# Kernel optimization log

Measured on AMD Instinct MI355X. Metric: run time of the kernel, lower is better.

Reference implementation:

```python
import jax, jax.numpy as jnp
import numpy as np

WIDTH = 64
MODES = 64
NBLOCKS = 4
PAD = 2
DT = 1.0
FSTRENGTH = 2.0
FORDER = 8


def _phi1(z, eps=1e-6):
    small = jnp.abs(z) < eps
    series = 1.0 + z * 0.5 + z * z / 6.0
    safe = (jnp.exp(z) - 1.0) / jnp.where(small, 1.0, z)
    return jnp.where(small, series, safe)


def _smooth_filter(m, strength, order):
    g = jnp.linspace(0.0, 1.0, m)
    r = jnp.sqrt(g * g + 1e-12)
    return jnp.exp(-strength * r ** order)


def setup_inputs() -> dict:
    key = jax.random.key(0)
    ks = jax.random.split(key, 12)
    B, X, IS, NC = 16, 16384, 10, 3
    W, M, NB = WIDTH, MODES, NBLOCKS
    H = 2 * W
    inp = {}
    inp["x"] = jax.random.normal(ks[0], (B, X, IS * NC), jnp.float32)
    inp["grid"] = jax.random.uniform(ks[1], (B, X, 1), jnp.float32)
    def lin(k, o, i):
        return jax.random.normal(k, (o, i), jnp.float32) / np.sqrt(i).astype(np.float32)
    inp["fc0_w"] = lin(ks[2], W, IS * NC + 1); inp["fc0_b"] = jnp.zeros((W,), jnp.float32)
    inp["fc1_w"] = lin(ks[3], 128, W); inp["fc1_b"] = jnp.zeros((128,), jnp.float32)
    inp["fc2_w"] = lin(ks[4], NC, 128); inp["fc2_b"] = jnp.zeros((NC,), jnp.float32)
    inp["g_w1"] = jax.random.normal(ks[5], (NB, H, W), jnp.float32) / np.sqrt(W).astype(np.float32)
    inp["g_b1"] = jnp.zeros((NB, H), jnp.float32)
    inp["g_w2"] = jax.random.normal(ks[6], (NB, W, H), jnp.float32) / np.sqrt(H).astype(np.float32)
    inp["g_b2"] = jnp.zeros((NB, W), jnp.float32)
    inp["w_w"] = jax.random.normal(ks[7], (NB, W, W), jnp.float32) / np.sqrt(W).astype(np.float32)
    inp["w_b"] = jnp.zeros((NB, W), jnp.float32)
    inp["log_decay"] = jax.random.normal(ks[8], (NB, W, M), jnp.float32) * 0.1
    scale = 1.0 / (W * W)
    inp["mix_re"] = scale * jax.random.uniform(ks[9], (NB, W, W, M), jnp.float32)
    inp["mix_im"] = scale * jax.random.uniform(ks[10], (NB, W, W, M), jnp.float32)
    inp["alpha_w_raw"] = jnp.asarray(np.log(np.expm1(0.6)), jnp.float32)
    inp["alpha_g_raw"] = jnp.asarray(np.log(np.expm1(1.0)), jnp.float32)
    return inp


def reference(x, grid, fc0_w, fc0_b, fc1_w, fc1_b, fc2_w, fc2_b,
              g_w1, g_b1, g_w2, g_b2, w_w, w_b, log_decay, mix_re, mix_im,
              alpha_w_raw, alpha_g_raw):
    gelu = lambda t: jax.nn.gelu(t, approximate=False)  # torch default GELU is exact erf
    # lift: cat grid, fc0, move channels first, pad right
    h = jnp.concatenate([x, grid], axis=-1) @ fc0_w.T + fc0_b      # [B,X,W]
    h = jnp.transpose(h, (0, 2, 1))                                 # [B,W,X]
    h = jnp.pad(h, ((0, 0), (0, 0), (0, PAD)))                      # [B,W,Xp]
    Xp = h.shape[-1]
    aw = jax.nn.softplus(alpha_w_raw)
    ag = jax.nn.softplus(alpha_g_raw)
    filt = _smooth_filter(MODES, FSTRENGTH, FORDER)                 # [M]
    for i in range(NBLOCKS):
        # pointwise MLP g(x) (1x1 convs == channel matmuls)
        gmid = gelu(jnp.einsum('oc,bcx->box', g_w1[i], h) + g_b1[i][None, :, None])
        g = ag * (jnp.einsum('oc,bcx->box', g_w2[i], gmid) + g_b2[i][None, :, None])
        # spectral ETD step
        v_hat = jnp.fft.rfft(h)                                     # [B,W,Xp//2+1] complex
        g_hat = jnp.fft.rfft(g)
        lam = -jax.nn.softplus(log_decay[i])                        # [W,M], beta=0 so real
        z = DT * lam
        expz = jnp.exp(z)[None]                                     # [1,W,M]
        phi = _phi1(z)[None]
        mix = mix_re[i] + 1j * mix_im[i]                            # [W,W,M]
        gm = jnp.einsum('bim,iom->bom', g_hat[:, :, :MODES], mix)
        out_m = expz * v_hat[:, :, :MODES] + (DT * phi * gm) * filt[None, None, :]
        out_hat = jnp.concatenate([out_m, jnp.zeros_like(v_hat[:, :, MODES:])], axis=-1)
        etd_out = jnp.fft.irfft(out_hat, n=Xp)
        # skip path: 1x1 conv, scaled (inner_steps=1 -> w_scale=1)
        wout = jnp.einsum('oc,bcx->box', w_w[i], h) + w_b[i][None, :, None]
        upd = etd_out + aw * wout
        h = upd if i == NBLOCKS - 1 else gelu(upd)
    h = h[..., :-PAD]
    h = jnp.transpose(h, (0, 2, 1))                                 # [B,X,W]
    h = gelu(h @ fc1_w.T + fc1_b)
    h = h @ fc2_w.T + fc2_b
    return h[:, :, None, :]                                         # [B,X,1,NC]
```

## Files before the change

kernel.cpp:

```cpp
#include <hip/hip_runtime.h>
#include <hip/hip_bf16.h>


#define BB 16
#define X 16384
#define XP 16386
#define XPAD 16512
#define W 64
#define H 128
#define M 64
#define NB 4
#define NC 3

typedef __hip_bfloat16 bf16;
typedef __attribute__((ext_vector_type(8))) short short8;
typedef __attribute__((ext_vector_type(4))) float floatx4;

__device__ __forceinline__ float gelu_f(float x){
  float x3 = x * x * x;
  float y2 = 1.5957691216f * x + 0.0713548162f * x3;
  float e = __expf(y2);
  float th = 1.f - 2.f / (e + 1.f);
  return 0.5f * x * (1.f + th);
}
__device__ __forceinline__ float softplus_f(float v){
  return (v > 20.f) ? v : log1pf(expf(v));
}
__device__ __forceinline__ short f2bs(float f){
  union { float f; unsigned u; } v; v.f = f;
  unsigned r = (v.u + 0x7FFFu + ((v.u >> 16) & 1u)) >> 16;
  return (short)r;
}
__device__ __forceinline__ float bs2f(short s){
  union { unsigned u; float f; } v; v.u = ((unsigned)(unsigned short)s) << 16;
  return v.f;
}
#define MFMA(a,b,c) __builtin_amdgcn_mfma_f32_16x16x32_bf16((a),(b),(c),0,0,0)

__global__ __launch_bounds__(256) void k_basisT(short* __restrict__ basT16){
  int idx = blockIdx.x * 256 + threadIdx.x;
  if (idx >= 128 * XPAD) return;
  int mp = idx / XPAD, x = idx - mp * XPAD;
  float v = 0.f;
  if (x < XP){
    int m = mp >> 1;
    int tt = (int)(((long long)x * (long long)m) % XP);
    float ang = 6.283185307179586477f * (float)tt / (float)XP;
    float s, c; sincosf(ang, &s, &c);
    v = (mp & 1) ? s : c;
  }
  basT16[idx] = f2bs(v);
}
__global__ __launch_bounds__(256) void k_basisC(short* __restrict__ basC16){
  int idx = blockIdx.x * 256 + threadIdx.x;
  if (idx >= XPAD * 128) return;
  int x = idx >> 7, kp = idx & 127;
  float v = 0.f;
  if (x < XP){
    int m = kp >> 1;
    int tt = (int)(((long long)x * (long long)m) % XP);
    float ang = 6.283185307179586477f * (float)tt / (float)XP;
    float s, c; sincosf(ang, &s, &c);
    v = (kp & 1) ? -s : c;
  }
  basC16[idx] = f2bs(v);
}

__global__ __launch_bounds__(256) void k_decay(const float* __restrict__ log_decay,
                                               float* __restrict__ expz,
                                               float* __restrict__ phi){
  int idx = blockIdx.x * 256 + threadIdx.x;
  if (idx >= NB * W * M) return;
  float z = -softplus_f(log_decay[idx]);
  expz[idx] = expf(z);
  float p;
  if (fabsf(z) < 1e-6f) p = 1.0f + 0.5f * z + z * z * (1.0f / 6.0f);
  else                  p = expm1f(z) / z;
  phi[idx] = p;
}

__global__ void k_filt(float* __restrict__ filt){
  int m = threadIdx.x;
  if (m < M){
    float g = (float)m / 63.0f;
    float r2 = g * g + 1e-12f;
    float r4 = r2 * r2;
    float r8 = r4 * r4;
    filt[m] = expf(-2.0f * r8);
  }
}

__global__ __launch_bounds__(256) void k_prep(const float* __restrict__ w_w,
                                              const float* __restrict__ g_w1,
                                              const float* __restrict__ fc1_w,
                                              const float* __restrict__ fc0_w,
                                              const float* __restrict__ awr,
                                              short* __restrict__ ww16,
                                              short* __restrict__ w116,
                                              short* __restrict__ w1fc16,
                                              short* __restrict__ w0fc16){
  int idx = blockIdx.x * 256 + threadIdx.x;
  float aw = softplus_f(awr[0]);
  if (idx < 16384){ ww16[idx] = f2bs(aw * w_w[idx]); }
  else if (idx < 49152){ int i = idx - 16384; w116[i] = f2bs(g_w1[i]); }
  else if (idx < 57344){ int i = idx - 49152; w1fc16[i] = f2bs(fc1_w[i]); }
  else if (idx < 59392){
    int i = idx - 57344;
    int o = i >> 5, f = i & 31;
    w0fc16[i] = (f < 31) ? f2bs(fc0_w[o * 31 + f]) : (short)0;
  }
}

__global__ __launch_bounds__(256) void k_fc0m(const float* __restrict__ xg,
                                              const float* __restrict__ gg,
                                              const short* __restrict__ w0fc16,
                                              const float* __restrict__ bg,
                                              short* __restrict__ h16,
                                              short* __restrict__ hX){
  __shared__ short xs16[128][40];
  __shared__ short xp[128][72];
  int b = blockIdx.y, bx = blockIdx.x, x0 = bx * 128, t = threadIdx.x;
  if (bx == 128){
    for (int i = t; i < 64 * 128; i += 256){
      int c = i >> 7, x = i & 127;
      h16[((size_t)b * 64 + c) * XPAD + x0 + x] = 0;
    }
    short8 z8 = (short8){0,0,0,0,0,0,0,0};
    for (int u = 0; u < 4; ++u){
      int idx = u * 256 + t;
      int x = idx >> 3, col = (idx & 7) * 8;
      *(short8*)&hX[((size_t)b * XPAD + x0 + x) * 64 + col] = z8;
    }
    return;
  }
  for (int i = t; i < 3840; i += 256){
    int x = i / 30, f = i - x * 30;
    xs16[x][f] = f2bs(xg[((size_t)b * X + x0 + x) * 30 + f]);
  }
  if (t < 128){ xs16[t][30] = f2bs(gg[(size_t)b * X + x0 + t]); xs16[t][31] = 0; }
  __syncthreads();
  int w = t >> 6, l = t & 63, q = l >> 4, ln = l & 15;
  floatx4 acc[4][2];
  #pragma unroll
  for (int mt = 0; mt < 4; ++mt)
    #pragma unroll
    for (int nt = 0; nt < 2; ++nt) acc[mt][nt] = (floatx4){0.f,0.f,0.f,0.f};
  #pragma unroll
  for (int mt = 0; mt < 4; ++mt){
    short8 av = *(const short8*)&w0fc16[(mt * 16 + ln) * 32 + q * 8];
    #pragma unroll
    for (int nt = 0; nt < 2; ++nt){
      short8 bv = *(const short8*)&xs16[w * 32 + nt * 16 + ln][q * 8];
      acc[mt][nt] = MFMA(av, bv, acc[mt][nt]);
    }
  }
  #pragma unroll
  for (int mt = 0; mt < 4; ++mt)
    #pragma unroll
    for (int r = 0; r < 4; ++r){
      int o = mt * 16 + q * 4 + r;
      float bias = bg[o];
      #pragma unroll
      for (int nt = 0; nt < 2; ++nt){
        int xl = w * 32 + nt * 16 + ln;
        short s = f2bs(acc[mt][nt][r] + bias);
        h16[((size_t)b * 64 + o) * XPAD + x0 + xl] = s;
        xp[xl][o] = s;
      }
    }
  __syncthreads();
  #pragma unroll
  for (int u = 0; u < 4; ++u){
    int idx = u * 256 + t;
    int x = idx >> 3, col = (idx & 7) * 8;
    *(short8*)&hX[((size_t)b * XPAD + x0 + x) * 64 + col] = *(const short8*)&xp[x][col];
  }
}

__global__ __launch_bounds__(256) void k_dft(const short* __restrict__ h16,
                                             const short* __restrict__ hX,
                                             const short* __restrict__ w116,
                                             const float* __restrict__ b1g,
                                             const short* __restrict__ basT16,
                                             float* __restrict__ vhat,
                                             float* __restrict__ gmidhat, int blk){
  __shared__ __align__(16) char smem[52224];
  short (*srcT)[136] = (short(*)[136])smem;
  short (*hT)[72]    = (short(*)[72])(smem + 17408);
  short (*basS)[136] = (short(*)[136])(smem + 17408);
  int b = blockIdx.y, z = blockIdx.z, bx = blockIdx.x, t = threadIdx.x;
  int w = t >> 6, l = t & 63, q = l >> 4, ln = l & 15;
  const short* hbase = h16 + (size_t)b * 64 * XPAD;
  const short* hXb   = hX + (size_t)b * XPAD * 64;
  floatx4 acc[8];
  #pragma unroll
  for (int i = 0; i < 8; ++i) acc[i] = (floatx4){0.f,0.f,0.f,0.f};
  short8 aw1[2];
  float bias[4];
  if (z){
    #pragma unroll
    for (int ks = 0; ks < 2; ++ks)
      aw1[ks] = *(const short8*)&w116[((size_t)blk * H + (z-1)*64 + w*16 + ln) * 64 + ks*32 + q*8];
    #pragma unroll
    for (int r = 0; r < 4; ++r)
      bias[r] = b1g[blk * H + (z-1)*64 + w*16 + q*4 + r];
  }
  for (int ci = bx; ci < 129; ci += 17){
    int xc = ci * 128;
    __syncthreads();
    if (z == 0){
      #pragma unroll
      for (int u = 0; u < 4; ++u){
        int idx = u * 256 + t;
        int c = idx >> 4, col = (idx & 15) * 8;
        *(short8*)&srcT[c][col] = *(const short8*)&hbase[(size_t)c * XPAD + xc + col];
      }
    } else {
      #pragma unroll
      for (int u = 0; u < 4; ++u){
        int idx = u * 256 + t;
        int x = idx >> 3, col = (idx & 7) * 8;
        *(short8*)&hT[x][col] = *(const short8*)&hXb[(size_t)(xc + x) * 64 + col];
      }
    }
    __syncthreads();
    if (z){
      floatx4 a2[8];
      #pragma unroll
      for (int i = 0; i < 8; ++i) a2[i] = (floatx4){0.f,0.f,0.f,0.f};
      #pragma unroll
      for (int ks = 0; ks < 2; ++ks){
        #pragma unroll
        for (int nt = 0; nt < 8; ++nt){
          short8 bv = *(const short8*)&hT[nt*16 + ln][ks*32 + q*8];
          a2[nt] = MFMA(aw1[ks], bv, a2[nt]);
        }
      }
      #pragma unroll
      for (int nt = 0; nt < 8; ++nt){
        int gx = xc + nt*16 + ln;
        #pragma unroll
        for (int r = 0; r < 4; ++r){
          int o = w*16 + q*4 + r;
          float vv = gelu_f(a2[nt][r] + bias[r]);
          srcT[o][nt*16 + ln] = (gx < XP) ? f2bs(vv) : (short)0;
        }
      }
    }
    __syncthreads();
    #pragma unroll
    for (int u = 0; u < 8; ++u){
      int idx = u * 256 + t;
      int mp = idx >> 4, col = (idx & 15) * 8;
      *(short8*)&basS[mp][col] = *(const short8*)&basT16[(size_t)mp * XPAD + xc + col];
    }
    __syncthreads();
    #pragma unroll
    for (int ks = 0; ks < 4; ++ks){
      short8 av = *(const short8*)&srcT[w*16 + ln][ks*32 + q*8];
      #pragma unroll
      for (int nt = 0; nt < 8; ++nt){
        short8 bv = *(const short8*)&basS[nt*16 + ln][ks*32 + q*8];
        acc[nt] = MFMA(av, bv, acc[nt]);
      }
    }
  }
  #pragma unroll
  for (int nt = 0; nt < 8; ++nt)
    #pragma unroll
    for (int r = 0; r < 4; ++r){
      int mp = nt*16 + ln;
      int c  = w*16 + q*4 + r;
      float v = acc[nt][r];
      if (mp & 1) v = -v;
      if (z == 0) atomicAdd(&vhat[((size_t)b * W + c) * 128 + mp], v);
      else atomicAdd(&gmidhat[((size_t)b * H + (z-1)*64 + c) * 128 + mp], v);
    }
}

__global__ __launch_bounds__(256) void k_ghat(const float* __restrict__ gmidhat,
                                              const float* __restrict__ w2g,
                                              const float* __restrict__ b2g,
                                              const float* __restrict__ agr,
                                              float* __restrict__ ghat, int blk){
  __shared__ float w2s[64][133];
  int b = blockIdx.x, zg = blockIdx.y, t = threadIdx.x;
  float ag = softplus_f(agr[0]);
  for (int i = t; i < 8192; i += 256) w2s[i >> 7][i & 127] = w2g[(size_t)blk * 8192 + i];
  __syncthreads();
  int i = t & 63, ms = t >> 6;
  int mp0 = zg * 16 + ms * 4;
  for (int j = 0; j < 4; ++j){
    int mp = mp0 + j;
    float acc = 0.f;
    for (int c2 = 0; c2 < H; ++c2)
      acc = fmaf(w2s[i][c2], gmidhat[((size_t)b * H + c2) * 128 + mp], acc);
    if (mp == 0) acc += (float)XP * b2g[blk * W + i];
    ghat[((size_t)b * W + i) * 128 + mp] = ag * acc;
  }
}

__global__ __launch_bounds__(256) void k_outm(const float* __restrict__ vhat,
                       const float* __restrict__ ghat,
                       const float* __restrict__ mix_re, const float* __restrict__ mix_im,
                       const float* __restrict__ expz, const float* __restrict__ phi,
                       const float* __restrict__ filt, short* __restrict__ outm16, int blk){
  int b = blockIdx.y, t = threadIdx.x;
  int m = t & 63, os = t >> 6;
  int o = blockIdx.x * 4 + os;
  const float* mre = mix_re + (size_t)blk * W * W * M + (size_t)o * M + m;
  const float* mim = mix_im + (size_t)blk * W * W * M + (size_t)o * M + m;
  float gr = 0.f, gi = 0.f;
  for (int i = 0; i < W; ++i){
    float gre = ghat[((size_t)b * W + i) * 128 + 2 * m];
    float gim = ghat[((size_t)b * W + i) * 128 + 2 * m + 1];
    float xr = mre[(size_t)i * W * M];
    float xi = mim[(size_t)i * W * M];
    gr = fmaf(gre, xr, gr); gr = fmaf(-gim, xi, gr);
    gi = fmaf(gre, xi, gi); gi = fmaf( gim, xr, gi);
  }
  int om = blk * W * M + o * M + m;
  float ez = expz[om], ph = phi[om], fl = filt[m];
  float vr = vhat[((size_t)b * W + o) * 128 + 2 * m];
  float vi = vhat[((size_t)b * W + o) * 128 + 2 * m + 1];
  float outr = fmaf(ez, vr, ph * fl * gr);
  float outi = fmaf(ez, vi, ph * fl * gi);
  float sc = ((m == 0) ? 1.0f : 2.0f) / (float)XP;
  outm16[((size_t)b * W + o) * 128 + 2 * m]     = f2bs(outr * sc);
  outm16[((size_t)b * W + o) * 128 + 2 * m + 1] = f2bs(outi * sc);
}

__global__ __launch_bounds__(256) void k_update(short* __restrict__ h16,
                                                short* __restrict__ hX,
                                                const short* __restrict__ outm16,
                                                const short* __restrict__ basC16,
                                                const short* __restrict__ ww16,
                                                const float* __restrict__ wbg,
                                                const float* __restrict__ awr, int blk){
  __shared__ __align__(16) char smem[52224];
  short (*hT)[72]    = (short(*)[72])smem;
  short (*wwS)[72]   = (short(*)[72])(smem + 18432);
  short (*basS)[136] = (short(*)[136])smem;
  short (*omS)[136]  = (short(*)[136])(smem + 34816);
  short (*xp)[72]    = (short(*)[72])smem;
  int b = blockIdx.y, x0 = blockIdx.x * 128, t = threadIdx.x;
  int w = t >> 6, l = t & 63, q = l >> 4, ln = l & 15;
  float aw = softplus_f(awr[0]);
  const short* hXb = hX + (size_t)b * XPAD * 64;
  #pragma unroll
  for (int u = 0; u < 4; ++u){
    int idx = u * 256 + t;
    int x = idx >> 3, col = (idx & 7) * 8;
    *(short8*)&hT[x][col] = *(const short8*)&hXb[(size_t)(x0 + x) * 64 + col];
  }
  #pragma unroll
  for (int u = 0; u < 2; ++u){
    int idx = u * 256 + t;
    int o = idx >> 3, col = (idx & 7) * 8;
    *(short8*)&wwS[o][col] = *(const short8*)&ww16[((size_t)blk * W + o) * 64 + col];
  }
  __syncthreads();
  floatx4 acc[2][4];
  #pragma unroll
  for (int mt = 0; mt < 2; ++mt)
    #pragma unroll
    for (int nt = 0; nt < 4; ++nt) acc[mt][nt] = (floatx4){0.f,0.f,0.f,0.f};
  #pragma unroll
  for (int ks = 0; ks < 2; ++ks){
    short8 a0 = *(const short8*)&hT[(w*2+0)*16 + ln][ks*32 + q*8];
    short8 a1 = *(const short8*)&hT[(w*2+1)*16 + ln][ks*32 + q*8];
    #pragma unroll
    for (int nt = 0; nt < 4; ++nt){
      short8 bv = *(const short8*)&wwS[nt*16 + ln][ks*32 + q*8];
      acc[0][nt] = MFMA(a0, bv, acc[0][nt]);
      acc[1][nt] = MFMA(a1, bv, acc[1][nt]);
    }
  }
  __syncthreads();
  #pragma unroll
  for (int u = 0; u < 8; ++u){
    int idx = u * 256 + t;
    int x = idx >> 4, col = (idx & 15) * 8;
    *(short8*)&basS[x][col] = *(const short8*)&basC16[(size_t)(x0 + x) * 128 + col];
  }
  #pragma unroll
  for (int u = 0; u < 4; ++u){
    int idx = u * 256 + t;
    int o = idx >> 4, col = (idx & 15) * 8;
    *(short8*)&omS[o][col] = *(const short8*)&outm16[((size_t)b * W + o) * 128 + col];
  }
  __syncthreads();
  #pragma unroll
  for (int ks = 0; ks < 4; ++ks){
    short8 a0 = *(const short8*)&basS[(w*2+0)*16 + ln][ks*32 + q*8];
    short8 a1 = *(const short8*)&basS[(w*2+1)*16 + ln][ks*32 + q*8];
    #pragma unroll
    for (int nt = 0; nt < 4; ++nt){
      short8 bv = *(const short8*)&omS[nt*16 + ln][ks*32 + q*8];
      acc[0][nt] = MFMA(a0, bv, acc[0][nt]);
      acc[1][nt] = MFMA(a1, bv, acc[1][nt]);
    }
  }
  short sreg[2][4][4];
  #pragma unroll
  for (int mt = 0; mt < 2; ++mt)
    #pragma unroll
    for (int nt = 0; nt < 4; ++nt){
      int o = nt*16 + ln;
      int xbase = x0 + (w*2+mt)*16 + q*4;
      float wbv = aw * wbg[blk * W + o];
      short* hp = &h16[((size_t)b * 64 + o) * XPAD + xbase];
      #pragma unroll
      for (int r = 0; r < 4; ++r){
        float u = acc[mt][nt][r] + wbv;
        if (blk != NB - 1) u = gelu_f(u);
        sreg[mt][nt][r] = f2bs(u);
      }
      if (xbase + 3 < XP){
        *(short4*)hp = *(short4*)&sreg[mt][nt][0];
      } else {
        #pragma unroll
        for (int r = 0; r < 4; ++r)
          if (xbase + r < XP) hp[r] = sreg[mt][nt][r];
      }
    }
  __syncthreads();
  #pragma unroll
  for (int mt = 0; mt < 2; ++mt)
    #pragma unroll
    for (int nt = 0; nt < 4; ++nt){
      int o = nt*16 + ln;
      int xl = (w*2+mt)*16 + q*4;
      #pragma unroll
      for (int r = 0; r < 4; ++r) xp[xl + r][o] = sreg[mt][nt][r];
    }
  __syncthreads();
  #pragma unroll
  for (int u = 0; u < 4; ++u){
    int idx = u * 256 + t;
    int x = idx >> 3, col = (idx & 7) * 8;
    if (x0 + x < XP)
      *(short8*)&hX[((size_t)b * XPAD + x0 + x) * 64 + col] = *(const short8*)&xp[x][col];
  }
}

__global__ __launch_bounds__(256) void k_fc12(const short* __restrict__ hX,
                                              const short* __restrict__ w1fc16,
                                              const float* __restrict__ b1,
                                              const float* __restrict__ w2,
                                              const float* __restrict__ b2,
                                              float* __restrict__ out){
  __shared__ short hT[128][72];
  __shared__ short gT[128][136];
  __shared__ float w2s[NC][132];
  __shared__ float red[2][128][NC];
  int b = blockIdx.y, x0 = blockIdx.x * 128, t = threadIdx.x;
  int w = t >> 6, l = t & 63, q = l >> 4, ln = l & 15;
  const short* hXb = hX + (size_t)b * XPAD * 64;
  #pragma unroll
  for (int u = 0; u < 4; ++u){
    int idx = u * 256 + t;
    int x = idx >> 3, col = (idx & 7) * 8;
    *(short8*)&hT[x][col] = *(const short8*)&hXb[(size_t)(x0 + x) * 64 + col];
  }
  for (int i = t; i < NC * H; i += 256) w2s[i / H][i % H] = w2[i];
  __syncthreads();
  floatx4 acc[2][8];
  #pragma unroll
  for (int mt = 0; mt < 2; ++mt)
    #pragma unroll
    for (int nt = 0; nt < 8; ++nt) acc[mt][nt] = (floatx4){0.f,0.f,0.f,0.f};
  #pragma unroll
  for (int ks = 0; ks < 2; ++ks){
    short8 a0 = *(const short8*)&w1fc16[(size_t)((w*2+0)*16 + ln) * 64 + ks*32 + q*8];
    short8 a1 = *(const short8*)&w1fc16[(size_t)((w*2+1)*16 + ln) * 64 + ks*32 + q*8];
    #pragma unroll
    for (int nt = 0; nt < 8; ++nt){
      short8 bv = *(const short8*)&hT[nt*16 + ln][ks*32 + q*8];
      acc[0][nt] = MFMA(a0, bv, acc[0][nt]);
      acc[1][nt] = MFMA(a1, bv, acc[1][nt]);
    }
  }
  #pragma unroll
  for (int mt = 0; mt < 2; ++mt){
    float bvv[4];
    #pragma unroll
    for (int r = 0; r < 4; ++r) bvv[r] = b1[(w*2+mt)*16 + q*4 + r];
    #pragma unroll
    for (int nt = 0; nt < 8; ++nt){
      int x = nt*16 + ln;
      #pragma unroll
      for (int r = 0; r < 4; ++r)
        gT[x][(w*2+mt)*16 + q*4 + r] = f2bs(gelu_f(acc[mt][nt][r] + bvv[r]));
    }
  }
  __syncthreads();
  int x = t & 127, half = t >> 7;
  float a3[NC] = {0.f, 0.f, 0.f};
  for (int og = 0; og < 8; ++og){
    int o0 = half * 64 + og * 8;
    short8 gv = *(const short8*)&gT[x][o0];
    #pragma unroll
    for (int j = 0; j < 8; ++j){
      float gf = bs2f(gv[j]);
      #pragma unroll
      for (int n = 0; n < NC; ++n) a3[n] = fmaf(gf, w2s[n][o0 + j], a3[n]);
    }
  }
  #pragma unroll
  for (int n = 0; n < NC; ++n) red[half][x][n] = a3[n];
  __syncthreads();
  if (half == 0){
    #pragma unroll
    for (int n = 0; n < NC; ++n)
      out[((size_t)b * X + x0 + x) * NC + n] = red[0][x][n] + red[1][x][n] + b2[n];
  }
}

extern "C" void kernel_launch(void* const* d_in, const int* in_sizes, int n_in,
                              void* d_out, int out_size, void* d_ws, size_t ws_size,
                              hipStream_t stream){
  (void)in_sizes; (void)n_in; (void)out_size; (void)ws_size;
  const float* x        = (const float*)d_in[0];
  const float* grid     = (const float*)d_in[1];
  const float* fc0_w    = (const float*)d_in[2];
  const float* fc0_b    = (const float*)d_in[3];
  const float* fc1_w    = (const float*)d_in[4];
  const float* fc1_b    = (const float*)d_in[5];
  const float* fc2_w    = (const float*)d_in[6];
  const float* fc2_b    = (const float*)d_in[7];
  const float* g_w1     = (const float*)d_in[8];
  const float* g_b1     = (const float*)d_in[9];
  const float* g_w2     = (const float*)d_in[10];
  const float* g_b2     = (const float*)d_in[11];
  const float* w_w      = (const float*)d_in[12];
  const float* w_b      = (const float*)d_in[13];
  const float* log_dec  = (const float*)d_in[14];
  const float* mix_re   = (const float*)d_in[15];
  const float* mix_im   = (const float*)d_in[16];
  const float* a_w      = (const float*)d_in[17];
  const float* a_g      = (const float*)d_in[18];
  float* out = (float*)d_out;

  short* basC16 = (short*)d_ws;
  short* basT16 = basC16 + (size_t)XPAD * 128;
  short* h16    = basT16 + (size_t)128 * XPAD;
  short* hX     = h16 + (size_t)BB * 64 * XPAD;
  float* vhat   = (float*)(hX + (size_t)BB * XPAD * 64);
  float* gmidhat= vhat + (size_t)BB * W * 128;
  float* ghat   = gmidhat + (size_t)BB * H * 128;
  float* expz   = ghat + (size_t)BB * W * 128;
  float* phi    = expz + NB * W * M;
  float* filt   = phi + NB * W * M;
  short* outm16 = (short*)(filt + 64);
  short* ww16   = outm16 + (size_t)BB * W * 128;
  short* w116   = ww16 + NB * W * W;
  short* w1fc16 = w116 + NB * H * W;
  short* w0fc16 = w1fc16 + H * W;

  k_basisT<<<dim3((128 * XPAD + 255) / 256), 256, 0, stream>>>(basT16);
  k_basisC<<<dim3((XPAD * 128 + 255) / 256), 256, 0, stream>>>(basC16);
  k_decay<<<dim3((NB * W * M + 255) / 256), 256, 0, stream>>>(log_dec, expz, phi);
  k_filt<<<1, 64, 0, stream>>>(filt);
  k_prep<<<dim3(232), 256, 0, stream>>>(w_w, g_w1, fc1_w, fc0_w, a_w, ww16, w116, w1fc16, w0fc16);
  k_fc0m<<<dim3(129, BB), 256, 0, stream>>>(x, grid, w0fc16, fc0_b, h16, hX);

  for (int blk = 0; blk < NB; ++blk){
    hipMemsetAsync(vhat, 0, (size_t)(BB * W * 128 + BB * H * 128) * sizeof(float), stream);
    k_dft<<<dim3(17, BB, 3), 256, 0, stream>>>(h16, hX, w116, g_b1, basT16, vhat, gmidhat, blk);
    k_ghat<<<dim3(BB, 8), 256, 0, stream>>>(gmidhat, g_w2, g_b2, a_g, ghat, blk);
    k_outm<<<dim3(16, BB), 256, 0, stream>>>(vhat, ghat, mix_re, mix_im, expz, phi, filt, outm16, blk);
    k_update<<<dim3(XPAD / 128, BB), 256, 0, stream>>>(h16, hX, outm16, basC16, ww16, w_b, a_w, blk);
  }
  k_fc12<<<dim3(X / 128, BB), 256, 0, stream>>>(hX, w1fc16, fc1_b, fc2_w, fc2_b, out);
}
```

Baseline: 681.9 us.

## Pre-swizzle DFT basis into MFMA fragment order and read from global directly

The cosine/sine basis tables are now generated in the exact per-lane MFMA fragment order, so each lane loads its short8 operand straight from global memory. This removes the LDS staging copy and one barrier in both the forward DFT kernel and the inverse update kernel, and it shrinks their shared memory footprint, which may allow higher occupancy. In exchange, basis reads go through L2/global on every MFMA operand instead of LDS, and the basis buffers grow slightly to 129 full chunks.

```diff
diff --git a/kernel.cpp b/kernel.cpp
--- a/kernel.cpp
+++ b/kernel.cpp
@@ -37,10 +37,16 @@
 }
 #define MFMA(a,b,c) __builtin_amdgcn_mfma_f32_16x16x32_bf16((a),(b),(c),0,0,0)
 
-__global__ __launch_bounds__(256) void k_basisT(short* __restrict__ basT16){
+__global__ __launch_bounds__(256) void k_basisTF(short* __restrict__ basTF){
   int idx = blockIdx.x * 256 + threadIdx.x;
-  if (idx >= 128 * XPAD) return;
-  int mp = idx / XPAD, x = idx - mp * XPAD;
+  if (idx >= 129 * 16384) return;
+  int j  = idx & 7;
+  int l  = (idx >> 3) & 63;
+  int ks = (idx >> 9) & 3;
+  int nt = (idx >> 11) & 7;
+  int ci = idx >> 14;
+  int x  = ci * 128 + ks * 32 + (l >> 4) * 8 + j;
+  int mp = nt * 16 + (l & 15);
   float v = 0.f;
   if (x < XP){
     int m = mp >> 1;
@@ -49,12 +55,18 @@
     float s, c; sincosf(ang, &s, &c);
     v = (mp & 1) ? s : c;
   }
-  basT16[idx] = f2bs(v);
-}
-__global__ __launch_bounds__(256) void k_basisC(short* __restrict__ basC16){
+  basTF[idx] = f2bs(v);
+}
+__global__ __launch_bounds__(256) void k_basisCF(short* __restrict__ basCF){
   int idx = blockIdx.x * 256 + threadIdx.x;
-  if (idx >= XPAD * 128) return;
-  int x = idx >> 7, kp = idx & 127;
+  if (idx >= 129 * 16384) return;
+  int j   = idx & 7;
+  int l   = (idx >> 3) & 63;
+  int ks  = (idx >> 9) & 3;
+  int sub = (idx >> 11) & 7;
+  int ci  = idx >> 14;
+  int x   = ci * 128 + sub * 16 + (l & 15);
+  int kp  = ks * 32 + (l >> 4) * 8 + j;
   float v = 0.f;
   if (x < XP){
     int m = kp >> 1;
@@ -63,7 +75,7 @@
     float s, c; sincosf(ang, &s, &c);
     v = (kp & 1) ? -s : c;
   }
-  basC16[idx] = f2bs(v);
+  basCF[idx] = f2bs(v);
 }
 
 __global__ __launch_bounds__(256) void k_decay(const float* __restrict__ log_decay,
@@ -181,13 +193,12 @@
                                              const short* __restrict__ hX,
                                              const short* __restrict__ w116,
                                              const float* __restrict__ b1g,
-                                             const short* __restrict__ basT16,
+                                             const short* __restrict__ basTF,
                                              float* __restrict__ vhat,
                                              float* __restrict__ gmidhat, int blk){
-  __shared__ __align__(16) char smem[52224];
+  __shared__ __align__(16) char smem[35840];
   short (*srcT)[136] = (short(*)[136])smem;
   short (*hT)[72]    = (short(*)[72])(smem + 17408);
-  short (*basS)[136] = (short(*)[136])(smem + 17408);
   int b = blockIdx.y, z = blockIdx.z, bx = blockIdx.x, t = threadIdx.x;
   int w = t >> 6, l = t & 63, q = l >> 4, ln = l & 15;
   const short* hbase = h16 + (size_t)b * 64 * XPAD;
@@ -222,9 +233,7 @@
         int x = idx >> 3, col = (idx & 7) * 8;
         *(short8*)&hT[x][col] = *(const short8*)&hXb[(size_t)(xc + x) * 64 + col];
       }
-    }
-    __syncthreads();
-    if (z){
+      __syncthreads();
       floatx4 a2[8];
       #pragma unroll
       for (int i = 0; i < 8; ++i) a2[i] = (floatx4){0.f,0.f,0.f,0.f};
@@ -248,19 +257,13 @@
       }
     }
     __syncthreads();
-    #pragma unroll
-    for (int u = 0; u < 8; ++u){
-      int idx = u * 256 + t;
-      int mp = idx >> 4, col = (idx & 15) * 8;
-      *(short8*)&basS[mp][col] = *(const short8*)&basT16[(size_t)mp * XPAD + xc + col];
-    }
-    __syncthreads();
+    const short8* bf = (const short8*)(basTF + (size_t)ci * 16384);
     #pragma unroll
     for (int ks = 0; ks < 4; ++ks){
       short8 av = *(const short8*)&srcT[w*16 + ln][ks*32 + q*8];
       #pragma unroll
       for (int nt = 0; nt < 8; ++nt){
-        short8 bv = *(const short8*)&basS[nt*16 + ln][ks*32 + q*8];
+        short8 bv = bf[(nt*4 + ks)*64 + l];
         acc[nt] = MFMA(av, bv, acc[nt]);
       }
     }
@@ -333,17 +336,16 @@
 __global__ __launch_bounds__(256) void k_update(short* __restrict__ h16,
                                                 short* __restrict__ hX,
                                                 const short* __restrict__ outm16,
-                                                const short* __restrict__ basC16,
+                                                const short* __restrict__ basCF,
                                                 const short* __restrict__ ww16,
                                                 const float* __restrict__ wbg,
                                                 const float* __restrict__ awr, int blk){
-  __shared__ __align__(16) char smem[52224];
-  short (*hT)[72]    = (short(*)[72])smem;
-  short (*wwS)[72]   = (short(*)[72])(smem + 18432);
-  short (*basS)[136] = (short(*)[136])smem;
-  short (*omS)[136]  = (short(*)[136])(smem + 34816);
-  short (*xp)[72]    = (short(*)[72])smem;
-  int b = blockIdx.y, x0 = blockIdx.x * 128, t = threadIdx.x;
+  __shared__ __align__(16) char smem[27648];
+  short (*hT)[72]   = (short(*)[72])smem;
+  short (*wwS)[72]  = (short(*)[72])(smem + 18432);
+  short (*omS)[136] = (short(*)[136])smem;
+  short (*xp)[72]   = (short(*)[72])smem;
+  int b = blockIdx.y, ci = blockIdx.x, x0 = ci * 128, t = threadIdx.x;
   int w = t >> 6, l = t & 63, q = l >> 4, ln = l & 15;
   float aw = softplus_f(awr[0]);
   const short* hXb = hX + (size_t)b * XPAD * 64;
@@ -378,22 +380,17 @@
   }
   __syncthreads();
   #pragma unroll
-  for (int u = 0; u < 8; ++u){
-    int idx = u * 256 + t;
-    int x = idx >> 4, col = (idx & 15) * 8;
-    *(short8*)&basS[x][col] = *(const short8*)&basC16[(size_t)(x0 + x) * 128 + col];
-  }
-  #pragma unroll
   for (int u = 0; u < 4; ++u){
     int idx = u * 256 + t;
     int o = idx >> 4, col = (idx & 15) * 8;
     *(short8*)&omS[o][col] = *(const short8*)&outm16[((size_t)b * W + o) * 128 + col];
   }
   __syncthreads();
+  const short8* bcf = (const short8*)(basCF + (size_t)ci * 16384);
   #pragma unroll
   for (int ks = 0; ks < 4; ++ks){
-    short8 a0 = *(const short8*)&basS[(w*2+0)*16 + ln][ks*32 + q*8];
-    short8 a1 = *(const short8*)&basS[(w*2+1)*16 + ln][ks*32 + q*8];
+    short8 a0 = bcf[((w*2+0)*4 + ks)*64 + l];
+    short8 a1 = bcf[((w*2+1)*4 + ks)*64 + l];
     #pragma unroll
     for (int nt = 0; nt < 4; ++nt){
       short8 bv = *(const short8*)&omS[nt*16 + ln][ks*32 + q*8];
@@ -542,9 +539,9 @@
   const float* a_g      = (const float*)d_in[18];
   float* out = (float*)d_out;
 
-  short* basC16 = (short*)d_ws;
-  short* basT16 = basC16 + (size_t)XPAD * 128;
-  short* h16    = basT16 + (size_t)128 * XPAD;
+  short* basCF  = (short*)d_ws;
+  short* basTF  = basCF + (size_t)129 * 16384;
+  short* h16    = basTF + (size_t)129 * 16384;
   short* hX     = h16 + (size_t)BB * 64 * XPAD;
   float* vhat   = (float*)(hX + (size_t)BB * XPAD * 64);
   float* gmidhat= vhat + (size_t)BB * W * 128;
@@ -558,8 +555,8 @@
   short* w1fc16 = w116 + NB * H * W;
   short* w0fc16 = w1fc16 + H * W;
 
-  k_basisT<<<dim3((128 * XPAD + 255) / 256), 256, 0, stream>>>(basT16);
-  k_basisC<<<dim3((XPAD * 128 + 255) / 256), 256, 0, stream>>>(basC16);
+  k_basisTF<<<dim3((129 * 16384 + 255) / 256), 256, 0, stream>>>(basTF);
+  k_basisCF<<<dim3((129 * 16384 + 255) / 256), 256, 0, stream>>>(basCF);
   k_decay<<<dim3((NB * W * M + 255) / 256), 256, 0, stream>>>(log_dec, expz, phi);
   k_filt<<<1, 64, 0, stream>>>(filt);
   k_prep<<<dim3(232), 256, 0, stream>>>(w_w, g_w1, fc1_w, fc0_w, a_w, ww16, w116, w1fc16, w0fc16);
@@ -567,10 +564,10 @@
 
   for (int blk = 0; blk < NB; ++blk){
     hipMemsetAsync(vhat, 0, (size_t)(BB * W * 128 + BB * H * 128) * sizeof(float), stream);
-    k_dft<<<dim3(17, BB, 3), 256, 0, stream>>>(h16, hX, w116, g_b1, basT16, vhat, gmidhat, blk);
+    k_dft<<<dim3(17, BB, 3), 256, 0, stream>>>(h16, hX, w116, g_b1, basTF, vhat, gmidhat, blk);
     k_ghat<<<dim3(BB, 8), 256, 0, stream>>>(gmidhat, g_w2, g_b2, a_g, ghat, blk);
     k_outm<<<dim3(16, BB), 256, 0, stream>>>(vhat, ghat, mix_re, mix_im, expz, phi, filt, outm16, blk);
-    k_update<<<dim3(XPAD / 128, BB), 256, 0, stream>>>(h16, hX, outm16, basC16, ww16, w_b, a_w, blk);
+    k_update<<<dim3(XPAD / 128, BB), 256, 0, stream>>>(h16, hX, outm16, basCF, ww16, w_b, a_w, blk);
   }
   k_fc12<<<dim3(X / 128, BB), 256, 0, stream>>>(hX, w1fc16, fc1_b, fc2_w, fc2_b, out);
 }
```

New measurement: 938.0 us. 37.6% more time.
